# Kernel optimization log

Measured on AMD Instinct MI355X. Metric: run time of the kernel, lower is better.

The kernel has to match this reference:

```python
import jax, jax.numpy as jnp
from jax import lax
import numpy as np

N_SEGMENT = 8
N_DIV = 4
C = 256
NT = 64  # n_batch(8) * n_segment(8)
H = W = 56


def _ms_weights(planes, n_div):
    fold = planes // n_div
    w1 = np.zeros((planes, 1, 1, 1, 1), np.float32); w1[:, 0, 0] = 1.0
    w3 = np.zeros((planes, 1, 3, 1, 1), np.float32)
    w3[:fold, 0, 0] = 1.0; w3[fold:2 * fold, 0, 2] = 1.0; w3[2 * fold:, 0, 1] = 1.0
    w5 = np.zeros((planes, 1, 5, 1, 1), np.float32)
    w5[:fold, 0, :2] = 1.0; w5[fold:2 * fold, 0, 3:] = 1.0; w5[2 * fold:, 0, 2] = 1.0
    w7 = np.zeros((planes, 1, 7, 1, 1), np.float32)
    w7[:fold, 0, :3] = 1.0; w7[fold:2 * fold, 0, 4:] = 1.0; w7[2 * fold:, 0, 3] = 1.0
    return w1, w3, w5, w7


def setup_inputs() -> dict:
    key = jax.random.key(0)
    kx, kn = jax.random.split(key)
    x = jax.random.normal(kx, (NT, C, H, W), dtype=jnp.float32)
    w1, w3, w5, w7 = _ms_weights(C // 4, N_DIV)
    net_w = jax.random.normal(kn, (C, C, 1, 1), dtype=jnp.float32) * (1.0 / np.sqrt(C))
    return {
        "x": x,
        "w1": jnp.asarray(w1), "w3": jnp.asarray(w3),
        "w5": jnp.asarray(w5), "w7": jnp.asarray(w7),
        "net_w": net_w,
    }


def _dw_temporal_conv3d(x, w, pad):
    # x: (n, c4, T, h, w); w: (c4, 1, K, 1, 1) depthwise over temporal dim
    return lax.conv_general_dilated(
        x, w, window_strides=(1, 1, 1),
        padding=[(pad, pad), (0, 0), (0, 0)],
        dimension_numbers=("NCDHW", "OIDHW", "NCDHW"),
        feature_group_count=x.shape[1])


def reference(x, w1, w3, w5, w7, net_w):
    nt, c, h, wd = x.shape
    n = nt // N_SEGMENT
    c4 = c // 4
    # (nt,c,h,w) -> (n, c, T, h, w)
    xv = x.reshape(n, N_SEGMENT, c, h, wd).transpose(0, 2, 1, 3, 4)
    ws = (w1, w3, w5, w7)
    pads = (0, 1, 2, 3)
    ys = [_dw_temporal_conv3d(xv[:, i * c4:(i + 1) * c4], ws[i], pads[i])
          for i in range(4)]
    y = jnp.concatenate(ys, axis=1)                       # (n, c, T, h, w)
    y = y.transpose(0, 2, 1, 3, 4).reshape(nt, c, h, wd)  # back to (nt,c,h,w)
    # wrapped net: bias-free 1x1 Conv2d
    out = lax.conv_general_dilated(
        y, net_w, window_strides=(1, 1), padding="VALID",
        dimension_numbers=("NCHW", "OIHW", "NCHW"))
    return out
```

## Files before the change

### kernel.cpp

```cpp
#include <hip/hip_runtime.h>

#define HW 3136
#define C_ 256
#define T_ 8
#define NPOS 64
#define NBLK_PER_NT 49
#define YSTRIDE 40
#define KP 352
#define NKS 11
#define FLAGBIT 0x40000000

typedef __attribute__((ext_vector_type(8))) short bf16x8;
typedef __attribute__((ext_vector_type(4))) float f32x4;
typedef __attribute__((ext_vector_type(4))) unsigned int u32x4;
typedef __attribute__((ext_vector_type(4))) int i32x4;

__device__ __forceinline__ unsigned short f2bf(float f) {
  unsigned int u = __float_as_uint(f);
  u += 0x7FFF + ((u >> 16) & 1);
  return (unsigned short)(u >> 16);
}


__global__ void prep_table(const float* __restrict__ w1, const float* __restrict__ w3,
                           const float* __restrict__ w5, const float* __restrict__ w7,
                           int* __restrict__ slotC, float* __restrict__ slotW,
                           int* __restrict__ rowtab) {
  const int c = threadIdx.x;
  for (int s = c; s < KP; s += 256) {
    slotC[s] = 0;
    slotW[s] = 0.f;
    for (int t = 0; t < T_; ++t) rowtab[t * KP + s] = 0;
  }
  const int g = c >> 6, lc = c & 63, K = 2 * g + 1;
  const float* wsrc = (g == 0) ? w1 : (g == 1) ? w3 : (g == 2) ? w5 : w7;
  float w[3] = {0.f, 0.f, 0.f};
  int d[3] = {0, 0, 0};
  int cnt = 0;
  for (int k = 0; k < K && cnt < 3; ++k) {
    float v = wsrc[lc * K + k];
    if (v != 0.0f) { w[cnt] = v; d[cnt] = k - g; ++cnt; }
  }
  __shared__ int ps[256];
  ps[c] = cnt;
  __syncthreads();
  for (int dlt = 1; dlt < 256; dlt <<= 1) {
    int v = (c >= dlt) ? ps[c - dlt] : 0;
    __syncthreads();
    ps[c] += v;
    __syncthreads();
  }
  const int off = ps[c] - cnt;
  for (int i = 0; i < cnt; ++i) {
    const int s = off + i;
    if (s >= KP) break;
    slotC[s] = c;
    slotW[s] = w[i];
    for (int t = 0; t < T_; ++t) {
      const int tq = t + d[i];
      const bool valid = (unsigned)tq < (unsigned)T_;
      const int tqc = valid ? tq : (tq < 0 ? 0 : T_ - 1);
      rowtab[t * KP + s] = ((tqc * C_ + c) * HW) | (valid ? 0 : FLAGBIT);
    }
  }
}

__global__ void prep_wb(const float* __restrict__ net_w, const int* __restrict__ slotC,
                        const float* __restrict__ slotW, unsigned short* __restrict__ Wbp) {
  const int oc = blockIdx.x;
  const int s = threadIdx.x;
  if (s < KP) Wbp[oc * KP + s] = f2bf(net_w[oc * C_ + slotC[s]] * slotW[s]);
}

__global__ __launch_bounds__(256, 4) void fused_kernel(
    const float* __restrict__ x, const unsigned short* __restrict__ Wbp,
    const int* __restrict__ rowtab, float* __restrict__ out) {
  const int blk = blockIdx.x;
  const int nt = blk / NBLK_PER_NT;
  const int p0 = (blk % NBLK_PER_NT) * NPOS;
  const int n = nt >> 3, t = nt & 7;
  const int tid = threadIdx.x;
  const int lane = tid & 63;
  const int wv = tid >> 6;
  const int m16 = lane & 15;
  const int quad = lane >> 4;
  const int pp = tid & 63;
  const int chunk = tid >> 6;

  __shared__ __align__(16) unsigned short ylds[2][NPOS * YSTRIDE];
  __shared__ __align__(16) int ltab[KP];

  for (int i = tid; i < KP; i += 256) ltab[i] = rowtab[t * KP + i];

  f32x4 acc[4][4];
#pragma unroll
  for (int i = 0; i < 4; ++i)
#pragma unroll
    for (int j = 0; j < 4; ++j) acc[i][j] = (f32x4){0.f, 0.f, 0.f, 0.f};

  const float* xn = x + (size_t)(n * 8) * C_ * HW + (size_t)(p0 + pp);

  __syncthreads();

  float xv[2][8];
  {
    const i32x4 o0 = *(const i32x4*)&ltab[chunk * 8];
    const i32x4 o1 = *(const i32x4*)&ltab[chunk * 8 + 4];
#pragma unroll
    for (int j = 0; j < 4; ++j) {
      const int ofa = o0[j];
      const float va = xn[ofa & (FLAGBIT - 1)];
      xv[0][j] = (ofa & FLAGBIT) ? 0.f : va;
      const int ofb = o1[j];
      const float vb = xn[ofb & (FLAGBIT - 1)];
      xv[0][4 + j] = (ofb & FLAGBIT) ? 0.f : vb;
    }
  }

#pragma unroll
  for (int ks = 0; ks < NKS; ++ks) {
    const int buf = ks & 1;
    bf16x8 af[4];
#pragma unroll
    for (int mi = 0; mi < 4; ++mi)
      af[mi] = *(const bf16x8*)&Wbp[(size_t)((wv * 64 + mi * 16 + m16) * KP) + ks * 32 + quad * 8];
    unsigned short pk[8];
#pragma unroll
    for (int j = 0; j < 8; ++j) pk[j] = f2bf(xv[buf][j]);
    *(u32x4*)&ylds[buf][pp * YSTRIDE + chunk * 8] = *(const u32x4*)pk;
    if (ks + 1 < NKS) {
      const i32x4 o0 = *(const i32x4*)&ltab[(ks + 1) * 32 + chunk * 8];
      const i32x4 o1 = *(const i32x4*)&ltab[(ks + 1) * 32 + chunk * 8 + 4];
#pragma unroll
      for (int j = 0; j < 4; ++j) {
        const int ofa = o0[j];
        const float va = xn[ofa & (FLAGBIT - 1)];
        xv[buf ^ 1][j] = (ofa & FLAGBIT) ? 0.f : va;
        const int ofb = o1[j];
        const float vb = xn[ofb & (FLAGBIT - 1)];
        xv[buf ^ 1][4 + j] = (ofb & FLAGBIT) ? 0.f : vb;
      }
    }
    __syncthreads();
#pragma unroll
    for (int ni = 0; ni < 4; ++ni) {
      const bf16x8 bfrag = *(const bf16x8*)&ylds[buf][(ni * 16 + m16) * YSTRIDE + quad * 8];
#pragma unroll
      for (int mi = 0; mi < 4; ++mi)
        acc[mi][ni] =
            __builtin_amdgcn_mfma_f32_16x16x32_bf16(af[mi], bfrag, acc[mi][ni], 0, 0, 0);
    }
  }

  const size_t obase = (size_t)nt * C_ * HW + p0 + m16;
#pragma unroll
  for (int mi = 0; mi < 4; ++mi) {
#pragma unroll
    for (int r = 0; r < 4; ++r) {
      const int oc = wv * 64 + mi * 16 + quad * 4 + r;
      float* orow = out + obase + (size_t)oc * HW;
#pragma unroll
      for (int ni = 0; ni < 4; ++ni) orow[ni * 16] = acc[mi][ni][r];
    }
  }
}

extern "C" void kernel_launch(void* const* d_in, const int* in_sizes, int n_in,
                              void* d_out, int out_size, void* d_ws, size_t ws_size,
                              hipStream_t stream) {
  const float* x = (const float*)d_in[0];
  const float* w1 = (const float*)d_in[1];
  const float* w3 = (const float*)d_in[2];
  const float* w5 = (const float*)d_in[3];
  const float* w7 = (const float*)d_in[4];
  const float* net_w = (const float*)d_in[5];
  float* out = (float*)d_out;

  char* ws = (char*)d_ws;
  unsigned short* Wbp = (unsigned short*)ws;
  int* slotC = (int*)(ws + 180224);
  float* slotW = (float*)(ws + 181632);
  int* rowtab = (int*)(ws + 183040);

  hipLaunchKernelGGL(prep_table, dim3(1), dim3(256), 0, stream, w1, w3, w5, w7,
                     slotC, slotW, rowtab);
  hipLaunchKernelGGL(prep_wb, dim3(C_), dim3(384), 0, stream, net_w, slotC, slotW, Wbp);
  hipLaunchKernelGGL(fused_kernel, dim3(64 * NBLK_PER_NT), dim3(256), 0, stream,
                     x, Wbp, rowtab, out);
}
```

Baseline: 407.5 us.

## Deepen x-gather prefetch to two stages and use a barrier that skips vmcnt waits

The global gather of x values now runs two k-steps ahead using a triple register buffer instead of one step ahead. The __syncthreads is replaced by an explicit lgkmcnt(0) wait plus s_barrier wrapped in sched_barriers, so the barrier no longer waits for outstanding global loads. This keeps more memory requests in flight to hide latency. The extra registers led to lowering the occupancy hint from 4 to 3 blocks per CU, which may reduce latency hiding across waves.

```diff
diff --git a/kernel.cpp b/kernel.cpp
--- a/kernel.cpp
+++ b/kernel.cpp
@@ -72,7 +72,7 @@
   if (s < KP) Wbp[oc * KP + s] = f2bf(net_w[oc * C_ + slotC[s]] * slotW[s]);
 }
 
-__global__ __launch_bounds__(256, 4) void fused_kernel(
+__global__ __launch_bounds__(256, 3) void fused_kernel(
     const float* __restrict__ x, const unsigned short* __restrict__ Wbp,
     const int* __restrict__ rowtab, float* __restrict__ out) {
   const int blk = blockIdx.x;
@@ -102,23 +102,28 @@
 
   __syncthreads();
 
-  float xv[2][8];
-  {
-    const i32x4 o0 = *(const i32x4*)&ltab[chunk * 8];
-    const i32x4 o1 = *(const i32x4*)&ltab[chunk * 8 + 4];
-#pragma unroll
-    for (int j = 0; j < 4; ++j) {
-      const int ofa = o0[j];
-      const float va = xn[ofa & (FLAGBIT - 1)];
-      xv[0][j] = (ofa & FLAGBIT) ? 0.f : va;
-      const int ofb = o1[j];
-      const float vb = xn[ofb & (FLAGBIT - 1)];
-      xv[0][4 + j] = (ofb & FLAGBIT) ? 0.f : vb;
-    }
-  }
+#define LOADX(KS, DST)                                          \
+  do {                                                          \
+    const i32x4 o0 = *(const i32x4*)&ltab[(KS) * 32 + chunk * 8];      \
+    const i32x4 o1 = *(const i32x4*)&ltab[(KS) * 32 + chunk * 8 + 4];  \
+    _Pragma("unroll") for (int j = 0; j < 4; ++j) {             \
+      const int ofa = o0[j];                                    \
+      const float va = xn[ofa & (FLAGBIT - 1)];                 \
+      (DST)[j] = (ofa & FLAGBIT) ? 0.f : va;                    \
+      const int ofb = o1[j];                                    \
+      const float vb = xn[ofb & (FLAGBIT - 1)];                 \
+      (DST)[4 + j] = (ofb & FLAGBIT) ? 0.f : vb;                \
+    }                                                           \
+  } while (0)
+
+  float xv[3][8];
+  LOADX(0, xv[0]);
+  LOADX(1, xv[1]);
 
 #pragma unroll
   for (int ks = 0; ks < NKS; ++ks) {
+    const int cur = ks % 3;
+    const int nxt = (ks + 2) % 3;
     const int buf = ks & 1;
     bf16x8 af[4];
 #pragma unroll
@@ -126,22 +131,13 @@
       af[mi] = *(const bf16x8*)&Wbp[(size_t)((wv * 64 + mi * 16 + m16) * KP) + ks * 32 + quad * 8];
     unsigned short pk[8];
 #pragma unroll
-    for (int j = 0; j < 8; ++j) pk[j] = f2bf(xv[buf][j]);
+    for (int j = 0; j < 8; ++j) pk[j] = f2bf(xv[cur][j]);
     *(u32x4*)&ylds[buf][pp * YSTRIDE + chunk * 8] = *(const u32x4*)pk;
-    if (ks + 1 < NKS) {
-      const i32x4 o0 = *(const i32x4*)&ltab[(ks + 1) * 32 + chunk * 8];
-      const i32x4 o1 = *(const i32x4*)&ltab[(ks + 1) * 32 + chunk * 8 + 4];
-#pragma unroll
-      for (int j = 0; j < 4; ++j) {
-        const int ofa = o0[j];
-        const float va = xn[ofa & (FLAGBIT - 1)];
-        xv[buf ^ 1][j] = (ofa & FLAGBIT) ? 0.f : va;
-        const int ofb = o1[j];
-        const float vb = xn[ofb & (FLAGBIT - 1)];
-        xv[buf ^ 1][4 + j] = (ofb & FLAGBIT) ? 0.f : vb;
-      }
-    }
-    __syncthreads();
+    if (ks + 2 < NKS) LOADX(ks + 2, xv[nxt]);
+    __builtin_amdgcn_sched_barrier(0);
+    asm volatile("s_waitcnt lgkmcnt(0)" ::: "memory");
+    __builtin_amdgcn_s_barrier();
+    __builtin_amdgcn_sched_barrier(0);
 #pragma unroll
     for (int ni = 0; ni < 4; ++ni) {
       const bf16x8 bfrag = *(const bf16x8*)&ylds[buf][(ni * 16 + m16) * YSTRIDE + quad * 8];
@@ -151,6 +147,7 @@
             __builtin_amdgcn_mfma_f32_16x16x32_bf16(af[mi], bfrag, acc[mi][ni], 0, 0, 0);
     }
   }
+#undef LOADX
 
   const size_t obase = (size_t)nt * C_ * HW + p0 + m16;
 #pragma unroll
```

Result: faster. 396.4 us (-2.7%).
